# Kernel tuning notes

Hardware: AMD Instinct MI355X
Metric: run time of the kernel (lower is better)

Reference implementation:

```python
import jax, jax.numpy as jnp
import numpy as np

EPS_ALPHA = 1e-7
EPS_STEP = 1e-6


def setup_inputs() -> dict:
    key = jax.random.key(0)
    k1, k2, k3 = jax.random.split(key, 3)
    B, T, D = 32, 1024, 512
    x = jax.random.normal(k1, (B, T, D), dtype=jnp.float32)
    # Linear(in_dim, 1) params (sigmoid-gain init approximated with small normal)
    W = jax.random.normal(k2, (D, 1), dtype=jnp.float32) * (1.0 / np.sqrt(D))
    b = jnp.zeros((1,), dtype=jnp.float32)
    return {"x": x, "W": W, "b": b, "r": 1, "num_steps": 1024}


def reference(x, W, b, r, num_steps):
    # x: [B, T, D]; r is unused (as in the original forward)
    B, T, D = x.shape
    speeds = jax.nn.sigmoid(jnp.einsum('btd,do->bto', x, W) + b)  # [B, T, 1]
    sp = speeds[:, :, 0]  # [B, T]

    # alpha0 = [1, 1e-7, 1e-7, ...]
    alpha0 = jnp.concatenate(
        [jnp.ones((B, 1), x.dtype), jnp.full((B, T - 1), EPS_ALPHA, x.dtype)], axis=1)

    def step(alpha, _):
        # u = alpha . speeds  -> [B, 1]
        u = jnp.sum(alpha * sp, axis=1, keepdims=True)
        sq = 1.7 - jnp.abs(u - 0.5)  # 1 + 0.7 - |u-0.5|
        shifted = jnp.pad(alpha[:, :-1], ((0, 0), (1, 0)))  # forward shift
        a = ((1.0 - u) * alpha + u * shifted + EPS_STEP) ** sq
        a = a / jnp.sum(a, axis=1, keepdims=True)
        return a, a

    _, alphas = jax.lax.scan(step, alpha0, None, length=num_steps)  # [S, B, T]
    alphas = jnp.transpose(alphas, (1, 0, 2))  # [B, S, T]
    contexts = jnp.einsum('bst,btd->bsd', alphas, x)  # [B, S, D]
    return contexts, alphas
```

## Files before the change

### kernel.cpp

```cpp
#include <hip/hip_runtime.h>
#include <hip/hip_bf16.h>

#define NB 32
#define NT 1024
#define ND 512
#define NS 1024

#define CTX_ELEMS (32u * 1024u * 512u)
#define SP_SCRATCH_OFF (CTX_ELEMS - 32u*1024u)

__device__ __forceinline__ float vlog2(float x) {
    float r; asm("v_log_f32 %0, %1" : "=v"(r) : "v"(x)); return r;
}
__device__ __forceinline__ float vexp2(float x) {
    float r; asm("v_exp_f32 %0, %1" : "=v"(r) : "v"(x)); return r;
}
__device__ __forceinline__ float vrcp(float x) {
    float r; asm("v_rcp_f32 %0, %1" : "=v"(r) : "v"(x)); return r;
}

template<int ctrl, int rm, int bm, bool bc>
__device__ __forceinline__ float dppadd(float x) {
    int y = __builtin_amdgcn_update_dpp(0, __float_as_int(x), ctrl, rm, bm, bc);
    return x + __int_as_float(y);
}
__device__ __forceinline__ float reduce63(float x) {
    x = dppadd<0x111, 0xf, 0xf, true >(x);
    x = dppadd<0x112, 0xf, 0xf, true >(x);
    x = dppadd<0x114, 0xf, 0xf, true >(x);
    x = dppadd<0x118, 0xf, 0xf, true >(x);
    x = dppadd<0x142, 0xa, 0xf, false>(x);
    x = dppadd<0x143, 0xc, 0xf, false>(x);
    return x;
}
__device__ __forceinline__ float wave_shr1(float x) {
    int y = __builtin_amdgcn_update_dpp(0, __float_as_int(x), 0x138, 0xf, 0xf, true);
    return __int_as_float(y);
}

__device__ __forceinline__ void lds_barrier() {
    asm volatile("s_waitcnt lgkmcnt(0)" ::: "memory");
    __builtin_amdgcn_s_barrier();
    asm volatile("" ::: "memory");
}

__global__ __launch_bounds__(256) void sp_kernel(const float* __restrict__ x,
                                                 const float* __restrict__ W,
                                                 const float* __restrict__ bias,
                                                 float* __restrict__ sp)
{
    const int lane = threadIdx.x & 63;
    const int wid  = threadIdx.x >> 6;
    const int row  = blockIdx.x * 4 + wid;
    const float4* xr = reinterpret_cast<const float4*>(x + (size_t)row * ND) + lane * 2;
    const float4* wr = reinterpret_cast<const float4*>(W) + lane * 2;
    float4 xa = xr[0], xb = xr[1];
    float4 wa = wr[0], wb = wr[1];
    float d = xa.x*wa.x + xa.y*wa.y + xa.z*wa.z + xa.w*wa.w
            + xb.x*wb.x + xb.y*wb.y + xb.z*wb.z + xb.w*wb.w;
    #pragma unroll
    for (int m = 1; m < 64; m <<= 1) d += __shfl_xor(d, m);
    if (lane == 0) {
        float z = d + bias[0];
        float e = vexp2(-z * 1.442695040888963f);
        sp[row] = 1.0f / (1.0f + e);
    }
}

__global__ __launch_bounds__(256) void scan_kernel(const float* __restrict__ sp,
                                                   float* __restrict__ alphas)
{
    const int b    = blockIdx.x;
    const int tx   = threadIdx.x;
    const int lane = tx & 63;
    const int wid  = tx >> 6;

    __shared__ float r1[2][4];
    __shared__ float r2[2][4];
    __shared__ float rb[2][4];

    float spv[4], raw[4];
    {
        float4 v = *reinterpret_cast<const float4*>(sp + (size_t)b * NT + tx * 4);
        spv[0] = v.x; spv[1] = v.y; spv[2] = v.z; spv[3] = v.w;
    }
    #pragma unroll
    for (int j = 0; j < 4; ++j) raw[j] = 1e-7f;
    if (tx == 0) raw[0] = 1.0f;
    float carry = (wid == 0) ? 0.0f : 1e-7f;

    {
        float p2 = fmaf(raw[0], spv[0], fmaf(raw[1], spv[1], fmaf(raw[2], spv[2], raw[3]*spv[3])));
        p2 = reduce63(p2);
        if (lane == 63) r2[1][wid] = p2;
    }
    __syncthreads();
    float u;
    {
        float4 v2 = *reinterpret_cast<const float4*>(r2[1]);
        u = (v2.x + v2.y) + (v2.z + v2.w);
    }
    float inv = 1.0f;

    float* outp = alphas + (size_t)b * NS * NT + tx * 4;

    for (int s = 0; s < NS; ++s) {
        const int p = s & 1;
        const float sq = 1.7f - fabsf(u - 0.5f);
        const float c1 = (1.0f - u) * inv;
        const float c0 = u * inv;

        float prev = wave_shr1(raw[3]);
        float sh0  = (lane == 0) ? carry : prev;

        float anew[4];
        {
            float v0 = fmaf(c1, raw[0], fmaf(c0, sh0,    1e-6f));
            float v1 = fmaf(c1, raw[1], fmaf(c0, raw[0], 1e-6f));
            float v2 = fmaf(c1, raw[2], fmaf(c0, raw[1], 1e-6f));
            float v3 = fmaf(c1, raw[3], fmaf(c0, raw[2], 1e-6f));
            anew[0] = vexp2(sq * vlog2(v0));
            anew[1] = vexp2(sq * vlog2(v1));
            anew[2] = vexp2(sq * vlog2(v2));
            anew[3] = vexp2(sq * vlog2(v3));
        }

        float p1 = (anew[0] + anew[1]) + (anew[2] + anew[3]);
        float p2 = fmaf(anew[0], spv[0], anew[1]*spv[1]) + fmaf(anew[2], spv[2], anew[3]*spv[3]);
        p1 = reduce63(p1);
        p2 = reduce63(p2);
        if (lane == 63) { r1[p][wid] = p1; r2[p][wid] = p2; rb[p][wid] = anew[3]; }
        __syncthreads();

        float4 v1 = *reinterpret_cast<const float4*>(r1[p]);
        float4 v2 = *reinterpret_cast<const float4*>(r2[p]);
        float bc  = rb[p][(wid == 0) ? 0 : (wid - 1)];
        carry = (wid == 0) ? 0.0f : bc;

        float t1 = (v1.x + v1.y) + (v1.z + v1.w);
        float t2 = (v2.x + v2.y) + (v2.z + v2.w);
        inv = vrcp(t1);
        u   = t2 * inv;

        float4 o;
        o.x = anew[0] * inv; o.y = anew[1] * inv; o.z = anew[2] * inv; o.w = anew[3] * inv;
        *reinterpret_cast<float4*>(outp + (size_t)s * NT) = o;

        #pragma unroll
        for (int j = 0; j < 4; ++j) raw[j] = anew[j];
    }
}

typedef __bf16 bf16x8 __attribute__((ext_vector_type(8)));
typedef float  f32x4  __attribute__((ext_vector_type(4)));

#define BM 256
#define BN 256
#define BK 32
#define LDP 40

__global__ __launch_bounds__(512, 2) void gemm_kernel(const float* __restrict__ alphas,
                                                      const float* __restrict__ x,
                                                      float* __restrict__ contexts)
{
    __shared__ __align__(16) __bf16 As[BM * LDP];
    __shared__ __align__(16) __bf16 Xs[BN * LDP];

    const int b  = blockIdx.z;
    const int s0 = blockIdx.y * BM;
    const int n0 = blockIdx.x * BN;
    const int tx = threadIdx.x;
    const int lane = tx & 63;
    const int wid  = tx >> 6;
    const int wm = wid >> 2;
    const int wn = wid & 3;
    const int lr = lane & 15;
    const int lk = (lane >> 4) * 8;

    f32x4 acc[8][4];
    #pragma unroll
    for (int i = 0; i < 8; ++i)
        #pragma unroll
        for (int j = 0; j < 4; ++j) acc[i][j] = (f32x4){0.f, 0.f, 0.f, 0.f};

    const int arow = tx >> 1;
    const int akb  = (tx & 1) * 16;
    const int xk0 = tx >> 6;
    const int xn4 = (tx & 63) * 4;

    const float* ap = alphas + ((size_t)b * NS + s0 + arow) * NT + akb;
    const float* xp = x + ((size_t)b * NT + xk0) * ND + n0 + xn4;

    float4 va0 = reinterpret_cast<const float4*>(ap)[0];
    float4 va1 = reinterpret_cast<const float4*>(ap)[1];
    float4 va2 = reinterpret_cast<const float4*>(ap)[2];
    float4 va3 = reinterpret_cast<const float4*>(ap)[3];
    float4 vx0 = *reinterpret_cast<const float4*>(xp + 0 * 8 * ND);
    float4 vx1 = *reinterpret_cast<const float4*>(xp + 1 * 8 * ND);
    float4 vx2 = *reinterpret_cast<const float4*>(xp + 2 * 8 * ND);
    float4 vx3 = *reinterpret_cast<const float4*>(xp + 3 * 8 * ND);
    ap += BK;
    xp += (size_t)BK * ND;

    for (int k0 = 0; k0 < NT; k0 += BK) {
        {
            bf16x8 w0, w1;
            w0[0]=(__bf16)va0.x; w0[1]=(__bf16)va0.y; w0[2]=(__bf16)va0.z; w0[3]=(__bf16)va0.w;
            w0[4]=(__bf16)va1.x; w0[5]=(__bf16)va1.y; w0[6]=(__bf16)va1.z; w0[7]=(__bf16)va1.w;
            w1[0]=(__bf16)va2.x; w1[1]=(__bf16)va2.y; w1[2]=(__bf16)va2.z; w1[3]=(__bf16)va2.w;
            w1[4]=(__bf16)va3.x; w1[5]=(__bf16)va3.y; w1[6]=(__bf16)va3.z; w1[7]=(__bf16)va3.w;
            *reinterpret_cast<bf16x8*>(&As[arow * LDP + akb])     = w0;
            *reinterpret_cast<bf16x8*>(&As[arow * LDP + akb + 8]) = w1;
            Xs[(xn4+0)*LDP + xk0]      = (__bf16)vx0.x;
            Xs[(xn4+1)*LDP + xk0]      = (__bf16)vx0.y;
            Xs[(xn4+2)*LDP + xk0]      = (__bf16)vx0.z;
            Xs[(xn4+3)*LDP + xk0]      = (__bf16)vx0.w;
            Xs[(xn4+0)*LDP + xk0 + 8]  = (__bf16)vx1.x;
            Xs[(xn4+1)*LDP + xk0 + 8]  = (__bf16)vx1.y;
            Xs[(xn4+2)*LDP + xk0 + 8]  = (__bf16)vx1.z;
            Xs[(xn4+3)*LDP + xk0 + 8]  = (__bf16)vx1.w;
            Xs[(xn4+0)*LDP + xk0 + 16] = (__bf16)vx2.x;
            Xs[(xn4+1)*LDP + xk0 + 16] = (__bf16)vx2.y;
            Xs[(xn4+2)*LDP + xk0 + 16] = (__bf16)vx2.z;
            Xs[(xn4+3)*LDP + xk0 + 16] = (__bf16)vx2.w;
            Xs[(xn4+0)*LDP + xk0 + 24] = (__bf16)vx3.x;
            Xs[(xn4+1)*LDP + xk0 + 24] = (__bf16)vx3.y;
            Xs[(xn4+2)*LDP + xk0 + 24] = (__bf16)vx3.z;
            Xs[(xn4+3)*LDP + xk0 + 24] = (__bf16)vx3.w;
        }
        if (k0 + BK < NT) {
            va0 = reinterpret_cast<const float4*>(ap)[0];
            va1 = reinterpret_cast<const float4*>(ap)[1];
            va2 = reinterpret_cast<const float4*>(ap)[2];
            va3 = reinterpret_cast<const float4*>(ap)[3];
            vx0 = *reinterpret_cast<const float4*>(xp + 0 * 8 * ND);
            vx1 = *reinterpret_cast<const float4*>(xp + 1 * 8 * ND);
            vx2 = *reinterpret_cast<const float4*>(xp + 2 * 8 * ND);
            vx3 = *reinterpret_cast<const float4*>(xp + 3 * 8 * ND);
            ap += BK;
            xp += (size_t)BK * ND;
        }
        lds_barrier();

        bf16x8 av[8], bv[4];
        #pragma unroll
        for (int j = 0; j < 4; ++j)
            bv[j] = *reinterpret_cast<const bf16x8*>(&Xs[(wn*64 + j*16 + lr) * LDP + lk]);
        #pragma unroll
        for (int i = 0; i < 8; ++i)
            av[i] = *reinterpret_cast<const bf16x8*>(&As[(wm*128 + i*16 + lr) * LDP + lk]);
        #pragma unroll
        for (int i = 0; i < 8; ++i)
            #pragma unroll
            for (int j = 0; j < 4; ++j)
                acc[i][j] = __builtin_amdgcn_mfma_f32_16x16x32_bf16(av[i], bv[j], acc[i][j], 0, 0, 0);
        lds_barrier();
    }

    const int ccol = lr;
    const int crow = (lane >> 4) * 4;
    #pragma unroll
    for (int i = 0; i < 8; ++i) {
        #pragma unroll
        for (int j = 0; j < 4; ++j) {
            int col = n0 + wn*64 + j*16 + ccol;
            int rw  = s0 + wm*128 + i*16 + crow;
            #pragma unroll
            for (int r = 0; r < 4; ++r)
                contexts[((size_t)b * NS + rw + r) * ND + col] = acc[i][j][r];
        }
    }
}

extern "C" void kernel_launch(void* const* d_in, const int* in_sizes, int n_in,
                              void* d_out, int out_size, void* d_ws, size_t ws_size,
                              hipStream_t stream) {
    const float* x    = (const float*)d_in[0];
    const float* W    = (const float*)d_in[1];
    const float* bias = (const float*)d_in[2];
    float* contexts = (float*)d_out;
    float* alphas   = (float*)d_out + CTX_ELEMS;
    float* sp       = (float*)d_out + SP_SCRATCH_OFF;

    sp_kernel<<<dim3(NB * NT / 4), dim3(256), 0, stream>>>(x, W, bias, sp);
    scan_kernel<<<dim3(NB), dim3(256), 0, stream>>>(sp, alphas);
    gemm_kernel<<<dim3(ND / BN, NS / BM, NB), dim3(512), 0, stream>>>(alphas, x, contexts);
}
```

Measured before the change: 398.3 us.

## Fuse scan and GEMM into one launch with per-chunk flag handoff

Merges the scan and GEMM kernels into one launch. The first 32 blocks run the sequential alpha scan and publish a release flag after every 256 steps. The other 256 blocks each spin on their batch's flag until their 256-step row chunk is ready, then run the bf16 GEMM tile. The aim is to overlap GEMM work with the latency-bound scan instead of running them back to back. In exchange it adds a workspace memset, spin-waiting, and idle upper threads in scan blocks that only mirror barriers. It also relies on all blocks being co-resident and risks GEMM blocks slowing the scan when they share CUs.

```diff
diff --git a/kernel.cpp b/kernel.cpp
--- a/kernel.cpp
+++ b/kernel.cpp
@@ -67,90 +67,6 @@
     }
 }
 
-__global__ __launch_bounds__(256) void scan_kernel(const float* __restrict__ sp,
-                                                   float* __restrict__ alphas)
-{
-    const int b    = blockIdx.x;
-    const int tx   = threadIdx.x;
-    const int lane = tx & 63;
-    const int wid  = tx >> 6;
-
-    __shared__ float r1[2][4];
-    __shared__ float r2[2][4];
-    __shared__ float rb[2][4];
-
-    float spv[4], raw[4];
-    {
-        float4 v = *reinterpret_cast<const float4*>(sp + (size_t)b * NT + tx * 4);
-        spv[0] = v.x; spv[1] = v.y; spv[2] = v.z; spv[3] = v.w;
-    }
-    #pragma unroll
-    for (int j = 0; j < 4; ++j) raw[j] = 1e-7f;
-    if (tx == 0) raw[0] = 1.0f;
-    float carry = (wid == 0) ? 0.0f : 1e-7f;
-
-    {
-        float p2 = fmaf(raw[0], spv[0], fmaf(raw[1], spv[1], fmaf(raw[2], spv[2], raw[3]*spv[3])));
-        p2 = reduce63(p2);
-        if (lane == 63) r2[1][wid] = p2;
-    }
-    __syncthreads();
-    float u;
-    {
-        float4 v2 = *reinterpret_cast<const float4*>(r2[1]);
-        u = (v2.x + v2.y) + (v2.z + v2.w);
-    }
-    float inv = 1.0f;
-
-    float* outp = alphas + (size_t)b * NS * NT + tx * 4;
-
-    for (int s = 0; s < NS; ++s) {
-        const int p = s & 1;
-        const float sq = 1.7f - fabsf(u - 0.5f);
-        const float c1 = (1.0f - u) * inv;
-        const float c0 = u * inv;
-
-        float prev = wave_shr1(raw[3]);
-        float sh0  = (lane == 0) ? carry : prev;
-
-        float anew[4];
-        {
-            float v0 = fmaf(c1, raw[0], fmaf(c0, sh0,    1e-6f));
-            float v1 = fmaf(c1, raw[1], fmaf(c0, raw[0], 1e-6f));
-            float v2 = fmaf(c1, raw[2], fmaf(c0, raw[1], 1e-6f));
-            float v3 = fmaf(c1, raw[3], fmaf(c0, raw[2], 1e-6f));
-            anew[0] = vexp2(sq * vlog2(v0));
-            anew[1] = vexp2(sq * vlog2(v1));
-            anew[2] = vexp2(sq * vlog2(v2));
-            anew[3] = vexp2(sq * vlog2(v3));
-        }
-
-        float p1 = (anew[0] + anew[1]) + (anew[2] + anew[3]);
-        float p2 = fmaf(anew[0], spv[0], anew[1]*spv[1]) + fmaf(anew[2], spv[2], anew[3]*spv[3]);
-        p1 = reduce63(p1);
-        p2 = reduce63(p2);
-        if (lane == 63) { r1[p][wid] = p1; r2[p][wid] = p2; rb[p][wid] = anew[3]; }
-        __syncthreads();
-
-        float4 v1 = *reinterpret_cast<const float4*>(r1[p]);
-        float4 v2 = *reinterpret_cast<const float4*>(r2[p]);
-        float bc  = rb[p][(wid == 0) ? 0 : (wid - 1)];
-        carry = (wid == 0) ? 0.0f : bc;
-
-        float t1 = (v1.x + v1.y) + (v1.z + v1.w);
-        float t2 = (v2.x + v2.y) + (v2.z + v2.w);
-        inv = vrcp(t1);
-        u   = t2 * inv;
-
-        float4 o;
-        o.x = anew[0] * inv; o.y = anew[1] * inv; o.z = anew[2] * inv; o.w = anew[3] * inv;
-        *reinterpret_cast<float4*>(outp + (size_t)s * NT) = o;
-
-        #pragma unroll
-        for (int j = 0; j < 4; ++j) raw[j] = anew[j];
-    }
-}
-
 typedef __bf16 bf16x8 __attribute__((ext_vector_type(8)));
 typedef float  f32x4  __attribute__((ext_vector_type(4)));
 
@@ -159,17 +75,125 @@
 #define BK 32
 #define LDP 40
 
-__global__ __launch_bounds__(512, 2) void gemm_kernel(const float* __restrict__ alphas,
-                                                      const float* __restrict__ x,
-                                                      float* __restrict__ contexts)
+__global__ __launch_bounds__(512, 2) void fused_kernel(const float* __restrict__ sp,
+                                                       const float* __restrict__ x,
+                                                       float* __restrict__ alphas,
+                                                       float* __restrict__ contexts,
+                                                       int* __restrict__ flags)
 {
     __shared__ __align__(16) __bf16 As[BM * LDP];
     __shared__ __align__(16) __bf16 Xs[BN * LDP];
-
-    const int b  = blockIdx.z;
-    const int s0 = blockIdx.y * BM;
-    const int n0 = blockIdx.x * BN;
-    const int tx = threadIdx.x;
+    __shared__ float r1[2][4];
+    __shared__ float r2[2][4];
+    __shared__ float rb[2][4];
+
+    const int bid = blockIdx.x;
+    const int tx  = threadIdx.x;
+
+    if (bid < NB) {
+        const int b = bid;
+        if (tx >= 256) {
+            __syncthreads();
+            for (int s = 0; s < NS; ++s) {
+                __syncthreads();
+                if ((s & 255) == 255) __syncthreads();
+            }
+            return;
+        }
+        const int lane = tx & 63;
+        const int wid  = tx >> 6;
+
+        float spv[4], raw[4];
+        {
+            float4 v = *reinterpret_cast<const float4*>(sp + (size_t)b * NT + tx * 4);
+            spv[0] = v.x; spv[1] = v.y; spv[2] = v.z; spv[3] = v.w;
+        }
+        #pragma unroll
+        for (int j = 0; j < 4; ++j) raw[j] = 1e-7f;
+        if (tx == 0) raw[0] = 1.0f;
+        float carry = (wid == 0) ? 0.0f : 1e-7f;
+
+        {
+            float p2 = fmaf(raw[0], spv[0], fmaf(raw[1], spv[1], fmaf(raw[2], spv[2], raw[3]*spv[3])));
+            p2 = reduce63(p2);
+            if (lane == 63) r2[1][wid] = p2;
+        }
+        __syncthreads();
+        float u;
+        {
+            float4 v2 = *reinterpret_cast<const float4*>(r2[1]);
+            u = (v2.x + v2.y) + (v2.z + v2.w);
+        }
+        float inv = 1.0f;
+
+        float* outp = alphas + (size_t)b * NS * NT + tx * 4;
+
+        for (int s = 0; s < NS; ++s) {
+            const int p = s & 1;
+            const float sq = 1.7f - fabsf(u - 0.5f);
+            const float c1 = (1.0f - u) * inv;
+            const float c0 = u * inv;
+
+            float prev = wave_shr1(raw[3]);
+            float sh0  = (lane == 0) ? carry : prev;
+
+            float anew[4];
+            {
+                float v0 = fmaf(c1, raw[0], fmaf(c0, sh0,    1e-6f));
+                float v1 = fmaf(c1, raw[1], fmaf(c0, raw[0], 1e-6f));
+                float v2 = fmaf(c1, raw[2], fmaf(c0, raw[1], 1e-6f));
+                float v3 = fmaf(c1, raw[3], fmaf(c0, raw[2], 1e-6f));
+                anew[0] = vexp2(sq * vlog2(v0));
+                anew[1] = vexp2(sq * vlog2(v1));
+                anew[2] = vexp2(sq * vlog2(v2));
+                anew[3] = vexp2(sq * vlog2(v3));
+            }
+
+            float p1 = (anew[0] + anew[1]) + (anew[2] + anew[3]);
+            float p2 = fmaf(anew[0], spv[0], anew[1]*spv[1]) + fmaf(anew[2], spv[2], anew[3]*spv[3]);
+            p1 = reduce63(p1);
+            p2 = reduce63(p2);
+            if (lane == 63) { r1[p][wid] = p1; r2[p][wid] = p2; rb[p][wid] = anew[3]; }
+            __syncthreads();
+
+            float4 v1 = *reinterpret_cast<const float4*>(r1[p]);
+            float4 v2 = *reinterpret_cast<const float4*>(r2[p]);
+            float bc  = rb[p][(wid == 0) ? 0 : (wid - 1)];
+            carry = (wid == 0) ? 0.0f : bc;
+
+            float t1 = (v1.x + v1.y) + (v1.z + v1.w);
+            float t2 = (v2.x + v2.y) + (v2.z + v2.w);
+            inv = vrcp(t1);
+            u   = t2 * inv;
+
+            float4 o;
+            o.x = anew[0] * inv; o.y = anew[1] * inv; o.z = anew[2] * inv; o.w = anew[3] * inv;
+            *reinterpret_cast<float4*>(outp + (size_t)s * NT) = o;
+
+            #pragma unroll
+            for (int j = 0; j < 4; ++j) raw[j] = anew[j];
+
+            if ((s & 255) == 255) {
+                asm volatile("s_waitcnt vmcnt(0)" ::: "memory");
+                __syncthreads();
+                if (tx == 0)
+                    __hip_atomic_store(&flags[b], (s >> 8) + 1,
+                                       __ATOMIC_RELEASE, __HIP_MEMORY_SCOPE_AGENT);
+            }
+        }
+        return;
+    }
+
+    const int g  = bid - NB;
+    const int sb = g >> 6;
+    const int b  = (g & 63) >> 1;
+    const int nb = g & 1;
+    const int s0 = sb * BM;
+    const int n0 = nb * BN;
+
+    while (__hip_atomic_load(&flags[b], __ATOMIC_ACQUIRE, __HIP_MEMORY_SCOPE_AGENT) < sb + 1)
+        __builtin_amdgcn_s_sleep(2);
+
     const int lane = tx & 63;
     const int wid  = tx >> 6;
     const int wm = wid >> 2;
@@ -211,22 +235,23 @@
             w1[4]=(__bf16)va3.x; w1[5]=(__bf16)va3.y; w1[6]=(__bf16)va3.z; w1[7]=(__bf16)va3.w;
             *reinterpret_cast<bf16x8*>(&As[arow * LDP + akb])     = w0;
             *reinterpret_cast<bf16x8*>(&As[arow * LDP + akb + 8]) = w1;
-            Xs[(xn4+0)*LDP + xk0]      = (__bf16)vx0.x;
-            Xs[(xn4+1)*LDP + xk0]      = (__bf16)vx0.y;
-            Xs[(xn4+2)*LDP + xk0]      = (__bf16)vx0.z;
-            Xs[(xn4+3)*LDP + xk0]      = (__bf16)vx0.w;
-            Xs[(xn4+0)*LDP + xk0 + 8]  = (__bf16)vx1.x;
-            Xs[(xn4+1)*LDP + xk0 + 8]  = (__bf16)vx1.y;
-            Xs[(xn4+2)*LDP + xk0 + 8]  = (__bf16)vx1.z;
-            Xs[(xn4+3)*LDP + xk0 + 8]  = (__bf16)vx1.w;
-            Xs[(xn4+0)*LDP + xk0 + 16] = (__bf16)vx2.x;
-            Xs[(xn4+1)*LDP + xk0 + 16] = (__bf16)vx2.y;
-            Xs[(xn4+2)*LDP + xk0 + 16] = (__bf16)vx2.z;
-            Xs[(xn4+3)*LDP + xk0 + 16] = (__bf16)vx2.w;
-            Xs[(xn4+0)*LDP + xk0 + 24] = (__bf16)vx3.x;
-            Xs[(xn4+1)*LDP + xk0 + 24] = (__bf16)vx3.y;
-            Xs[(xn4+2)*LDP + xk0 + 24] = (__bf16)vx3.z;
-            Xs[(xn4+3)*LDP + xk0 + 24] = (__bf16)vx3.w;
+            const int xk = xk0;
+            Xs[(xn4+0)*LDP + xk]      = (__bf16)vx0.x;
+            Xs[(xn4+1)*LDP + xk]      = (__bf16)vx0.y;
+            Xs[(xn4+2)*LDP + xk]      = (__bf16)vx0.z;
+            Xs[(xn4+3)*LDP + xk]      = (__bf16)vx0.w;
+            Xs[(xn4+0)*LDP + xk + 8]  = (__bf16)vx1.x;
+            Xs[(xn4+1)*LDP + xk + 8]  = (__bf16)vx1.y;
+            Xs[(xn4+2)*LDP + xk + 8]  = (__bf16)vx1.z;
+            Xs[(xn4+3)*LDP + xk + 8]  = (__bf16)vx1.w;
+            Xs[(xn4+0)*LDP + xk + 16] = (__bf16)vx2.x;
+            Xs[(xn4+1)*LDP + xk + 16] = (__bf16)vx2.y;
+            Xs[(xn4+2)*LDP + xk + 16] = (__bf16)vx2.z;
+            Xs[(xn4+3)*LDP + xk + 16] = (__bf16)vx2.w;
+            Xs[(xn4+0)*LDP + xk + 24] = (__bf16)vx3.x;
+            Xs[(xn4+1)*LDP + xk + 24] = (__bf16)vx3.y;
+            Xs[(xn4+2)*LDP + xk + 24] = (__bf16)vx3.z;
+            Xs[(xn4+3)*LDP + xk + 24] = (__bf16)vx3.w;
         }
         if (k0 + BK < NT) {
             va0 = reinterpret_cast<const float4*>(ap)[0];
@@ -280,9 +305,12 @@
     const float* bias = (const float*)d_in[2];
     float* contexts = (float*)d_out;
     float* alphas   = (float*)d_out + CTX_ELEMS;
-    float* sp       = (float*)d_out + SP_SCRATCH_OFF;
-
+    int*   flags    = (int*)d_ws;
+    float* sp = (ws_size >= (size_t)(256 + NB * NT * 4))
+                    ? (float*)((char*)d_ws + 256)
+                    : (float*)d_out + SP_SCRATCH_OFF;
+
+    hipMemsetAsync(d_ws, 0, 256, stream);
     sp_kernel<<<dim3(NB * NT / 4), dim3(256), 0, stream>>>(x, W, bias, sp);
-    scan_kernel<<<dim3(NB), dim3(256), 0, stream>>>(sp, alphas);
-    gemm_kernel<<<dim3(ND / BN, NS / BM, NB), dim3(512), 0, stream>>>(alphas, x, contexts);
-}
+    fused_kernel<<<dim3(NB + 256), dim3(512), 0, stream>>>(sp, x, alphas, contexts, flags);
+}
```

New measurement: 556.6 us. +39.7%, slower.

## Replace scan barrier with tagged LDS mailbox spin and remap GEMM grid for XCD locality

Applied to the files above, without the earlier changes.

In the serial scan kernel, the per-step __syncthreads is replaced by a mailbox. Each wave's lane 63 writes a 16-byte record of its partial sums, boundary value and step tag, and every wave spins reading all four records until the tags match. This targets barrier latency on the 1024-step critical path, but relies on LDS write visibility and ordering across waves without a barrier. The GEMM launch is also flattened to a 1D grid with a block-index remap so blocks sharing the same batch's alphas and x tiles land on the same XCD for L2 reuse.

```diff
diff --git a/kernel.cpp b/kernel.cpp
--- a/kernel.cpp
+++ b/kernel.cpp
@@ -8,6 +8,8 @@
 
 #define CTX_ELEMS (32u * 1024u * 512u)
 #define SP_SCRATCH_OFF (CTX_ELEMS - 32u*1024u)
+
+typedef float f32x4 __attribute__((ext_vector_type(4)));
 
 __device__ __forceinline__ float vlog2(float x) {
     float r; asm("v_log_f32 %0, %1" : "=v"(r) : "v"(x)); return r;
@@ -75,9 +77,10 @@
     const int lane = tx & 63;
     const int wid  = tx >> 6;
 
-    __shared__ float r1[2][4];
-    __shared__ float r2[2][4];
-    __shared__ float rb[2][4];
+    __shared__ __align__(16) f32x4 mbox[2][4];
+    __shared__ float u0s[4];
+
+    if (tx < 8) mbox[tx >> 2][tx & 3] = (f32x4){0.f, 0.f, 0.f, 0.f};
 
     float spv[4], raw[4];
     {
@@ -92,20 +95,21 @@
     {
         float p2 = fmaf(raw[0], spv[0], fmaf(raw[1], spv[1], fmaf(raw[2], spv[2], raw[3]*spv[3])));
         p2 = reduce63(p2);
-        if (lane == 63) r2[1][wid] = p2;
+        if (lane == 63) u0s[wid] = p2;
     }
     __syncthreads();
-    float u;
-    {
-        float4 v2 = *reinterpret_cast<const float4*>(r2[1]);
-        u = (v2.x + v2.y) + (v2.z + v2.w);
-    }
+    float u = (u0s[0] + u0s[1]) + (u0s[2] + u0s[3]);
     float inv = 1.0f;
 
+    const unsigned base0 = (unsigned)(uintptr_t)&mbox[0][0];
+    const unsigned base1 = (unsigned)(uintptr_t)&mbox[1][0];
+    const unsigned woff0 = base0 + (wid << 4);
+    const unsigned woff1 = base1 + (wid << 4);
+
     float* outp = alphas + (size_t)b * NS * NT + tx * 4;
+    float tagf = 1.0f;
 
     for (int s = 0; s < NS; ++s) {
-        const int p = s & 1;
         const float sq = 1.7f - fabsf(u - 0.5f);
         const float c1 = (1.0f - u) * inv;
         const float c0 = u * inv;
@@ -129,16 +133,33 @@
         float p2 = fmaf(anew[0], spv[0], anew[1]*spv[1]) + fmaf(anew[2], spv[2], anew[3]*spv[3]);
         p1 = reduce63(p1);
         p2 = reduce63(p2);
-        if (lane == 63) { r1[p][wid] = p1; r2[p][wid] = p2; rb[p][wid] = anew[3]; }
-        __syncthreads();
-
-        float4 v1 = *reinterpret_cast<const float4*>(r1[p]);
-        float4 v2 = *reinterpret_cast<const float4*>(r2[p]);
-        float bc  = rb[p][(wid == 0) ? 0 : (wid - 1)];
-        carry = (wid == 0) ? 0.0f : bc;
-
-        float t1 = (v1.x + v1.y) + (v1.z + v1.w);
-        float t2 = (v2.x + v2.y) + (v2.z + v2.w);
+
+        const unsigned woff = (s & 1) ? woff1 : woff0;
+        const unsigned rbase = (s & 1) ? base1 : base0;
+        if (lane == 63) {
+            f32x4 rec;
+            rec.x = p1; rec.y = p2; rec.z = anew[3]; rec.w = tagf;
+            asm volatile("ds_write_b128 %0, %1" :: "v"(woff), "v"(rec) : "memory");
+        }
+
+        f32x4 r0, r1, r2, r3;
+        do {
+            asm volatile(
+                "ds_read_b128 %0, %4\n\t"
+                "ds_read_b128 %1, %4 offset:16\n\t"
+                "ds_read_b128 %2, %4 offset:32\n\t"
+                "ds_read_b128 %3, %4 offset:48\n\t"
+                "s_waitcnt lgkmcnt(0)"
+                : "=v"(r0), "=v"(r1), "=v"(r2), "=v"(r3)
+                : "v"(rbase) : "memory");
+        } while (r0.w != tagf || r1.w != tagf || r2.w != tagf || r3.w != tagf);
+        tagf += 1.0f;
+
+        float bc = (wid == 1) ? r0.z : (wid == 2) ? r1.z : (wid == 3) ? r2.z : 0.0f;
+        carry = bc;
+
+        float t1 = (r0.x + r1.x) + (r2.x + r3.x);
+        float t2 = (r0.y + r1.y) + (r2.y + r3.y);
         inv = vrcp(t1);
         u   = t2 * inv;
 
@@ -152,7 +173,6 @@
 }
 
 typedef __bf16 bf16x8 __attribute__((ext_vector_type(8)));
-typedef float  f32x4  __attribute__((ext_vector_type(4)));
 
 #define BM 256
 #define BN 256
@@ -166,9 +186,16 @@
     __shared__ __align__(16) __bf16 As[BM * LDP];
     __shared__ __align__(16) __bf16 Xs[BN * LDP];
 
-    const int b  = blockIdx.z;
-    const int s0 = blockIdx.y * BM;
-    const int n0 = blockIdx.x * BN;
+    const int bid  = blockIdx.x;
+    const int low3 = bid & 7;
+    const int slot = bid >> 3;
+    const int nb   = slot & 1;
+    const int pair = (slot >> 1) * 8 + low3;
+    const int b    = pair >> 2;
+    const int sbi  = pair & 3;
+    const int s0 = sbi * BM;
+    const int n0 = nb * BN;
+
     const int tx = threadIdx.x;
     const int lane = tx & 63;
     const int wid  = tx >> 6;
@@ -284,5 +311,5 @@
 
     sp_kernel<<<dim3(NB * NT / 4), dim3(256), 0, stream>>>(x, W, bias, sp);
     scan_kernel<<<dim3(NB), dim3(256), 0, stream>>>(sp, alphas);
-    gemm_kernel<<<dim3(ND / BN, NS / BM, NB), dim3(512), 0, stream>>>(alphas, x, contexts);
-}
+    gemm_kernel<<<dim3(256), dim3(512), 0, stream>>>(alphas, x, contexts);
+}
```

Measured after the change: 540.3 us. 1.36x slower.
